# Kernel optimization log

Measured on AMD Instinct MI355X. Metric: run time of the kernel, lower is better.

Reference implementation:

```python
import jax, jax.numpy as jnp
import numpy as np

NEG = -1e30  # finite stand-in for -inf in the sparse-softmax mask


def setup_inputs() -> dict:
    key = jax.random.key(0)
    kh, kwl, kwn, kn = jax.random.split(key, 4)
    B, S, D, E = 8, 4096, 1024, 64
    return {
        "h": jax.random.normal(kh, (B, S, D), dtype=jnp.float32),
        "Wl": jax.random.normal(kwl, (E, D), dtype=jnp.float32) * 0.02,
        "bl": jnp.zeros((E,), dtype=jnp.float32),
        "Wn": jax.random.normal(kwn, (E, D), dtype=jnp.float32) * 0.02,
        "bn": jnp.zeros((E,), dtype=jnp.float32),
        "noise": jax.random.normal(kn, (B, S, E), dtype=jnp.float32),
        "top_k": 2,
    }


def reference(h, Wl, bl, Wn, bn, noise, top_k):
    # logits, noise std: two small linears over the expert dim
    logits = jnp.einsum("bsd,ed->bse", h, Wl) + bl          # [B,S,E]
    std = jax.nn.softplus(jnp.einsum("bsd,ed->bse", h, Wn) + bn)
    noisy = logits + noise * std                              # [B,S,E]

    full_p = jax.nn.softmax(noisy, axis=-1)

    topk_vals, ix = jax.lax.top_k(noisy, top_k)               # [B,S,k]
    E = noisy.shape[-1]
    # scatter top-k values back into a -inf-filled tensor == mask non-topk
    mask = jax.nn.one_hot(ix, E, dtype=jnp.bool_).any(axis=-2)  # [B,S,E]
    sparse = jnp.where(mask, noisy, NEG)
    route_p = jax.nn.softmax(sparse, axis=-1)
    return route_p, ix, full_p
```

## Files before the change

### kernel.cpp

```cpp
#include <hip/hip_runtime.h>
#include <math.h>


#define DIM 1024
#define NEXP 64
#define CS 132
#define LOSCALE 2048.0f
#define INV_LOSCALE (1.0f / 2048.0f)
#define ABUF 8192
#define BUFSZ 24576

using half8v   = __attribute__((ext_vector_type(8)))  _Float16;
using floatx16 = __attribute__((ext_vector_type(16))) float;

#define MFMA32(a, b, c) __builtin_amdgcn_mfma_f32_32x32x16_f16((a), (b), (c), 0, 0, 0)

__device__ inline void gll16(const void* g, void* l) {
    __builtin_amdgcn_global_load_lds(
        (const __attribute__((address_space(1))) unsigned int*)g,
        (__attribute__((address_space(3))) unsigned int*)l, 16, 0, 0);
}

__global__ __launch_bounds__(512)
void prep_B(const float* __restrict__ Wl, const float* __restrict__ Wn,
            _Float16* __restrict__ Bp)
{
    const int idx = blockIdx.x * 512 + threadIdx.x;
    const int r  = idx >> 7;
    const int c2 = idx & 127;
    const float* W = (r < 64) ? (Wl + (size_t)r * DIM) : (Wn + (size_t)(r - 64) * DIM);
    float f[8];
    *(float4*)(f)     = *(const float4*)(W + c2 * 8);
    *(float4*)(f + 4) = *(const float4*)(W + c2 * 8 + 4);
    half8v hi, lo;
#pragma unroll
    for (int i = 0; i < 8; i++) {
        _Float16 hh = (_Float16)f[i];
        hi[i] = hh;
        lo[i] = (_Float16)((f[i] - (float)hh) * LOSCALE);
    }
    const int t = c2 >> 2, cf = c2 & 3, sw = r & 7;
    _Float16* base = Bp + ((size_t)t * 128 + r) * 64;
    *(half8v*)(base + ((cf ^ sw) << 3))       = hi;
    *(half8v*)(base + (((4 | cf) ^ sw) << 3)) = lo;
}

__global__ __launch_bounds__(256, 3)
void router_fused(const float* __restrict__ h, const _Float16* __restrict__ Bp,
                  const float* __restrict__ bl, const float* __restrict__ bn,
                  const float* __restrict__ noise,
                  float* __restrict__ outR, float* __restrict__ outIx,
                  float* __restrict__ outF)
{
    __shared__ __align__(16) char lds_raw[2 * BUFSZ];

    const int tid   = threadIdx.x;
    const int wv    = tid >> 6;
    const int lane  = tid & 63;
    const int row31 = lane & 31;
    const int oct   = lane >> 5;
    const int expg  = wv * 32;
    const int tok0  = blockIdx.x * 64;

    const int rS = tid >> 2, gS = tid & 3;
    const float* aSrc = h + (size_t)(tok0 + rS) * DIM + gS * 8;
    const int aWrow = rS * 128;
    const int wHi = ((gS ^ (rS & 7)) << 4);
    const int wLo = (((4 | gS) ^ (rS & 7)) << 4);

    const _Float16* bSrc = Bp + tid * 8;
    char* dB = lds_raw + ABUF + (tid << 4);

    const int rowA0 = row31 * 128;
    const int rowA1 = rowA0 + 32 * 128;
    const int rowB  = ABUF + (expg + row31) * 128;
    const int swA = (row31 & 7) << 4;
    const int swB = ((expg + row31) & 7) << 4;

    floatx16 acc1_0, acc2_0, acc1_1, acc2_1;
#pragma unroll
    for (int i = 0; i < 16; i++) { acc1_0[i] = 0.f; acc2_0[i] = 0.f;
                                   acc1_1[i] = 0.f; acc2_1[i] = 0.f; }

#define CVTW(dst) do {                                                         \
        float f_[8] = {a0v.x, a0v.y, a0v.z, a0v.w, a1v.x, a1v.y, a1v.z, a1v.w};\
        half8v hi_, lo_;                                                       \
        _Pragma("unroll")                                                      \
        for (int i_ = 0; i_ < 8; i_++) {                                       \
            _Float16 hh_ = (_Float16)f_[i_];                                   \
            hi_[i_] = hh_;                                                     \
            lo_[i_] = (_Float16)((f_[i_] - (float)hh_) * LOSCALE);             \
        }                                                                      \
        *(half8v*)((dst) + aWrow + wHi) = hi_;                                 \
        *(half8v*)((dst) + aWrow + wLo) = lo_;                                 \
    } while (0)

#define ISSUE_B(tt) do {                                                       \
        char* db_ = dB + ((tt) & 1) * BUFSZ;                                   \
        const _Float16* bs_ = bSrc + (size_t)(tt) * 8192;                      \
        gll16(bs_,        db_);                                                \
        gll16(bs_ + 2048, db_ + 4096);                                         \
        gll16(bs_ + 4096, db_ + 8192);                                         \
        gll16(bs_ + 6144, db_ + 12288);                                        \
    } while (0)

    float4 a0v = *(const float4*)(aSrc);
    float4 a1v = *(const float4*)(aSrc + 4);
    ISSUE_B(0);
    CVTW(lds_raw);
    a0v = *(const float4*)(aSrc + 32);
    a1v = *(const float4*)(aSrc + 36);
    __syncthreads();

    for (int t = 0; t < 32; t++) {
        char* nbuf = lds_raw + ((t + 1) & 1) * BUFSZ;
        if (t < 31) {
            CVTW(nbuf);
            ISSUE_B(t + 1);
        }
        if (t < 30) {
            a0v = *(const float4*)(aSrc + 32 * (t + 2));
            a1v = *(const float4*)(aSrc + 32 * (t + 2) + 4);
        }
        const char* base = lds_raw + (t & 1) * BUFSZ;
#pragma unroll
        for (int ks = 0; ks < 2; ks++) {
            const int hc = (ks * 2 + oct) << 4;
            const half8v aH0 = *(const half8v*)(base + rowA0 + (hc ^ swA));
            const half8v aL0 = *(const half8v*)(base + rowA0 + ((64 | hc) ^ swA));
            const half8v aH1 = *(const half8v*)(base + rowA1 + (hc ^ swA));
            const half8v aL1 = *(const half8v*)(base + rowA1 + ((64 | hc) ^ swA));
            const half8v bH  = *(const half8v*)(base + rowB + (hc ^ swB));
            const half8v bL  = *(const half8v*)(base + rowB + ((64 | hc) ^ swB));
            acc1_0 = MFMA32(aH0, bH, acc1_0);
            acc2_0 = MFMA32(aH0, bL, acc2_0);
            acc2_0 = MFMA32(aL0, bH, acc2_0);
            acc1_1 = MFMA32(aH1, bH, acc1_1);
            acc2_1 = MFMA32(aH1, bL, acc2_1);
            acc2_1 = MFMA32(aL1, bH, acc2_1);
        }
        __syncthreads();
    }
#undef ISSUE_B
#undef CVTW

    float* Cs = (float*)lds_raw;
#pragma unroll
    for (int i = 0; i < 16; i++) {
        const int rowt = (i & 3) + 8 * (i >> 2) + 4 * oct;
        Cs[rowt * CS + expg + row31]        = acc1_0[i] + acc2_0[i] * INV_LOSCALE;
        Cs[(32 + rowt) * CS + expg + row31] = acc1_1[i] + acc2_1[i] * INV_LOSCALE;
    }
    __syncthreads();

    const float blv = bl[lane];
    const float bnv = bn[lane];

    for (int t = wv; t < 64; t += 4) {
        const int gt = tok0 + t;
        float xr = Cs[t * CS + lane] + blv;
        float xf = Cs[t * CS + 64 + lane] + bnv;
        float nz = noise[(size_t)gt * NEXP + lane];

        float stdv = fmaxf(xf, 0.f) + log1pf(expf(-fabsf(xf)));
        float noisy = fmaf(nz, stdv, xr);

        float v = noisy; int idx = lane;
#pragma unroll
        for (int o = 32; o > 0; o >>= 1) {
            float ov = __shfl_xor(v, o, 64);
            int   oi = __shfl_xor(idx, o, 64);
            if (ov > v || (ov == v && oi < idx)) { v = ov; idx = oi; }
        }
        const float v1 = v; const int i1 = idx;

        float p = expf(noisy - v1);
        float s = p;
#pragma unroll
        for (int o = 32; o > 0; o >>= 1) s += __shfl_xor(s, o, 64);
        float fullp = p / s;

        v = (lane == i1) ? -INFINITY : noisy; idx = lane;
#pragma unroll
        for (int o = 32; o > 0; o >>= 1) {
            float ov = __shfl_xor(v, o, 64);
            int   oi = __shfl_xor(idx, o, 64);
            if (ov > v || (ov == v && oi < idx)) { v = ov; idx = oi; }
        }
        const float v2 = v; const int i2 = idx;

        float e2 = expf(v2 - v1);
        float den = 1.f + e2;
        float routep = (lane == i1) ? (1.f / den) : ((lane == i2) ? (e2 / den) : 0.f);

        outR[(size_t)gt * NEXP + lane] = routep;
        outF[(size_t)gt * NEXP + lane] = fullp;
        if (lane == 0) {
            outIx[(size_t)gt * 2 + 0] = (float)i1;
            outIx[(size_t)gt * 2 + 1] = (float)i2;
        }
    }
}

extern "C" void kernel_launch(void* const* d_in, const int* in_sizes, int n_in,
                              void* d_out, int out_size, void* d_ws, size_t ws_size,
                              hipStream_t stream) {
    const float* h     = (const float*)d_in[0];
    const float* Wl    = (const float*)d_in[1];
    const float* bl    = (const float*)d_in[2];
    const float* Wn    = (const float*)d_in[3];
    const float* bn    = (const float*)d_in[4];
    const float* noise = (const float*)d_in[5];
    float* out = (float*)d_out;

    const int M = in_sizes[0] / DIM;
    float* outR  = out;
    float* outIx = out + (size_t)M * NEXP;
    float* outF  = outIx + (size_t)M * 2;

    _Float16* Bp = (_Float16*)d_ws;

    prep_B<<<32, 512, 0, stream>>>(Wl, Wn, Bp);
    router_fused<<<M / 64, 256, 0, stream>>>(h, Bp, bl, bn, noise, outR, outIx, outF);
}
```

Before: 256.6 us.

## Deepen A-prefetch to two stages with manual waitcnt and barrier scheduling

Rewrites the K-loop so global loads of h run two tiles ahead, using alternating register sets unrolled by two. Explicit vmcnt/lgkmcnt waits and sched_barriers replace __syncthreads, so loads stay in flight across the barrier instead of being drained each iteration. The async B load is now issued before the A conversion. Launch bounds drop from 3 to 2 blocks per CU, which gives more registers per thread but may lower occupancy for this memory-bound kernel.

```diff
diff --git a/kernel.cpp b/kernel.cpp
--- a/kernel.cpp
+++ b/kernel.cpp
@@ -14,6 +14,13 @@
 using floatx16 = __attribute__((ext_vector_type(16))) float;
 
 #define MFMA32(a, b, c) __builtin_amdgcn_mfma_f32_32x32x16_f16((a), (b), (c), 0, 0, 0)
+
+#define WAITV2    asm volatile("s_waitcnt vmcnt(2)" ::: "memory")
+#define WAITV4    asm volatile("s_waitcnt vmcnt(4)" ::: "memory")
+#define WAITV0    asm volatile("s_waitcnt vmcnt(0)" ::: "memory")
+#define WAITLGKM0 asm volatile("s_waitcnt lgkmcnt(0)" ::: "memory")
+#define SCHED0    __builtin_amdgcn_sched_barrier(0)
+#define BAR       __builtin_amdgcn_s_barrier()
 
 __device__ inline void gll16(const void* g, void* l) {
     __builtin_amdgcn_global_load_lds(
@@ -45,7 +52,7 @@
     *(half8v*)(base + (((4 | cf) ^ sw) << 3)) = lo;
 }
 
-__global__ __launch_bounds__(256, 3)
+__global__ __launch_bounds__(256, 2)
 void router_fused(const float* __restrict__ h, const _Float16* __restrict__ Bp,
                   const float* __restrict__ bl, const float* __restrict__ bn,
                   const float* __restrict__ noise,
@@ -82,8 +89,9 @@
     for (int i = 0; i < 16; i++) { acc1_0[i] = 0.f; acc2_0[i] = 0.f;
                                    acc1_1[i] = 0.f; acc2_1[i] = 0.f; }
 
-#define CVTW(dst) do {                                                         \
-        float f_[8] = {a0v.x, a0v.y, a0v.z, a0v.w, a1v.x, a1v.y, a1v.z, a1v.w};\
+#define CVTW_SET(dst, A0, A1) do {                                             \
+        float f_[8] = {(A0).x, (A0).y, (A0).z, (A0).w,                         \
+                       (A1).x, (A1).y, (A1).z, (A1).w};                        \
         half8v hi_, lo_;                                                       \
         _Pragma("unroll")                                                      \
         for (int i_ = 0; i_ < 8; i_++) {                                       \
@@ -104,45 +112,75 @@
         gll16(bs_ + 6144, db_ + 12288);                                        \
     } while (0)
 
-    float4 a0v = *(const float4*)(aSrc);
-    float4 a1v = *(const float4*)(aSrc + 4);
+#define COMPUTE(BASEP) do {                                                    \
+        const char* cbase_ = (const char*)(BASEP);                             \
+        _Pragma("unroll")                                                      \
+        for (int ks = 0; ks < 2; ks++) {                                       \
+            const int hc = (ks * 2 + oct) << 4;                                \
+            const half8v aH0 = *(const half8v*)(cbase_ + rowA0 + (hc ^ swA));  \
+            const half8v aL0 = *(const half8v*)(cbase_ + rowA0 + ((64|hc)^swA));\
+            const half8v aH1 = *(const half8v*)(cbase_ + rowA1 + (hc ^ swA));  \
+            const half8v aL1 = *(const half8v*)(cbase_ + rowA1 + ((64|hc)^swA));\
+            const half8v bH  = *(const half8v*)(cbase_ + rowB + (hc ^ swB));   \
+            const half8v bL  = *(const half8v*)(cbase_ + rowB + ((64|hc)^swB));\
+            acc1_0 = MFMA32(aH0, bH, acc1_0);                                  \
+            acc2_0 = MFMA32(aH0, bL, acc2_0);                                  \
+            acc2_0 = MFMA32(aL0, bH, acc2_0);                                  \
+            acc1_1 = MFMA32(aH1, bH, acc1_1);                                  \
+            acc2_1 = MFMA32(aH1, bL, acc2_1);                                  \
+            acc2_1 = MFMA32(aL1, bH, acc2_1);                                  \
+        }                                                                      \
+    } while (0)
+
+#define BODY(t, A0, A1) do {                                                   \
+        ISSUE_B((t) + 1);                                                      \
+        SCHED0;                                                                \
+        CVTW_SET(lds_raw + (((t) + 1) & 1) * BUFSZ, A0, A1);                   \
+        A0 = *(const float4*)(aSrc + 32 * ((t) + 3));                          \
+        A1 = *(const float4*)(aSrc + 32 * ((t) + 3) + 4);                      \
+        COMPUTE(lds_raw + ((t) & 1) * BUFSZ);                                  \
+        WAITLGKM0; WAITV2; SCHED0;                                             \
+        BAR;                                                                   \
+    } while (0)
+
+    float4 a0e = *(const float4*)(aSrc);
+    float4 a1e = *(const float4*)(aSrc + 4);
     ISSUE_B(0);
-    CVTW(lds_raw);
-    a0v = *(const float4*)(aSrc + 32);
-    a1v = *(const float4*)(aSrc + 36);
+    CVTW_SET(lds_raw, a0e, a1e);
+    SCHED0;
+    float4 a0o = *(const float4*)(aSrc + 32);
+    float4 a1o = *(const float4*)(aSrc + 36);
+    a0e = *(const float4*)(aSrc + 64);
+    a1e = *(const float4*)(aSrc + 68);
+    WAITLGKM0; WAITV4; SCHED0;
+    BAR;
+
+    for (int tb = 0; tb < 14; ++tb) {
+        const int t0 = 2 * tb;
+        BODY(t0,     a0o, a1o);
+        BODY(t0 + 1, a0e, a1e);
+    }
+    BODY(28, a0o, a1o);
+
+    ISSUE_B(30);
+    SCHED0;
+    CVTW_SET(lds_raw, a0e, a1e);
+    COMPUTE(lds_raw + BUFSZ);
+    WAITLGKM0; WAITV0; SCHED0;
+    BAR;
+    ISSUE_B(31);
+    SCHED0;
+    CVTW_SET(lds_raw + BUFSZ, a0o, a1o);
+    COMPUTE(lds_raw);
+    WAITLGKM0; WAITV0; SCHED0;
+    BAR;
+    COMPUTE(lds_raw + BUFSZ);
     __syncthreads();
 
-    for (int t = 0; t < 32; t++) {
-        char* nbuf = lds_raw + ((t + 1) & 1) * BUFSZ;
-        if (t < 31) {
-            CVTW(nbuf);
-            ISSUE_B(t + 1);
-        }
-        if (t < 30) {
-            a0v = *(const float4*)(aSrc + 32 * (t + 2));
-            a1v = *(const float4*)(aSrc + 32 * (t + 2) + 4);
-        }
-        const char* base = lds_raw + (t & 1) * BUFSZ;
-#pragma unroll
-        for (int ks = 0; ks < 2; ks++) {
-            const int hc = (ks * 2 + oct) << 4;
-            const half8v aH0 = *(const half8v*)(base + rowA0 + (hc ^ swA));
-            const half8v aL0 = *(const half8v*)(base + rowA0 + ((64 | hc) ^ swA));
-            const half8v aH1 = *(const half8v*)(base + rowA1 + (hc ^ swA));
-            const half8v aL1 = *(const half8v*)(base + rowA1 + ((64 | hc) ^ swA));
-            const half8v bH  = *(const half8v*)(base + rowB + (hc ^ swB));
-            const half8v bL  = *(const half8v*)(base + rowB + ((64 | hc) ^ swB));
-            acc1_0 = MFMA32(aH0, bH, acc1_0);
-            acc2_0 = MFMA32(aH0, bL, acc2_0);
-            acc2_0 = MFMA32(aL0, bH, acc2_0);
-            acc1_1 = MFMA32(aH1, bH, acc1_1);
-            acc2_1 = MFMA32(aH1, bL, acc2_1);
-            acc2_1 = MFMA32(aL1, bH, acc2_1);
-        }
-        __syncthreads();
-    }
+#undef BODY
+#undef COMPUTE
 #undef ISSUE_B
-#undef CVTW
+#undef CVTW_SET
 
     float* Cs = (float*)lds_raw;
 #pragma unroll
```

After: 253.4 us. No clear change (-1.2%).
